# Kernel tuning notes

Hardware: AMD Instinct MI355X
Metric: run time of the kernel (lower is better)

The kernel has to match this reference:

```python
import jax, jax.numpy as jnp
import numpy as np
from jax import lax

NUM_EXPERT = 2   # top-k experts kept per image
N_EXPERTS = 4    # total experts


def setup_inputs() -> dict:
    key = jax.random.key(0)
    ks = jax.random.split(key, 4)
    B, C, H, W = 16, 64, 128, 128
    inputs = jax.random.normal(ks[0], (B, C, H, W), dtype=jnp.float32)
    k = jax.random.uniform(ks[1], (B, C, 1, 1), dtype=jnp.float32)
    gate_w = jax.random.normal(ks[2], (N_EXPERTS, C), dtype=jnp.float32) * (1.0 / np.sqrt(C))
    gate_b = jnp.zeros((N_EXPERTS,), dtype=jnp.float32)
    conv_w = jax.random.normal(ks[3], (N_EXPERTS, C, C, 3, 3), dtype=jnp.float32) * (1.0 / np.sqrt(C * 9))
    conv_b = jnp.zeros((N_EXPERTS, C), dtype=jnp.float32)
    return {"inputs": inputs, "k": k, "gate_w": gate_w, "gate_b": gate_b,
            "conv_w": conv_w, "conv_b": conv_b}


def _expert(x, k, w, b):
    # expert_i(x, k) = ReLU(Conv3x3_i(x) + b_i) * k   (FiLM-style conditioning)
    y = lax.conv_general_dilated(x, w, window_strides=(1, 1), padding='SAME',
                                 dimension_numbers=('NCHW', 'OIHW', 'NCHW'))
    return jax.nn.relu(y + b[None, :, None, None]) * k


def reference(inputs, k, gate_w, gate_b, conv_w, conv_b):
    B = inputs.shape[0]
    # gate: global average pool over HW, then linear C -> E
    pooled = inputs.mean(axis=(2, 3))                       # [B, C]
    logits = pooled @ gate_w.T + gate_b                     # [B, E]
    # softmax in float32 (matches F.softmax(..., dtype=torch.float))
    weights = jax.nn.softmax(logits.astype(jnp.float32), axis=1).astype(inputs.dtype)
    topk_w, topk_idx = lax.top_k(weights, NUM_EXPERT)       # [B, num_expert]
    # scatter top-k weights into a dense [B, E] mask (zeros elsewhere)
    exp_weights = jnp.zeros_like(weights).at[jnp.arange(B)[:, None], topk_idx].set(topk_w)
    # dense loop over ALL experts, weighted sum with mostly-zero weights
    out = inputs
    for i in range(N_EXPERTS):
        out = out + _expert(inputs, k, conv_w[i], conv_b[i]) * exp_weights[:, i, None, None, None]
    return out
```

## Files before the change

### kernel.cpp

```cpp
#include <hip/hip_runtime.h>

typedef __attribute__((ext_vector_type(8))) short bfrag8;
typedef __attribute__((ext_vector_type(4))) short bfrag4;
typedef __attribute__((ext_vector_type(16))) float f32x16;

#define B_ 16
#define C_ 64
#define H_ 128
#define W_ 128
#define E_ 4
#define HW_ (H_ * W_)

#define PLANE 2080
#define ROWB  16640
#define RGK 4

#define WT_ELEMS (4 * 9 * 2 * 4 * 64 * 8)
#define OFF_POOL (WT_ELEMS * 2)
#define OFF_EW   (OFF_POOL + 1024 * 4)
#define WS_NEEDED ((size_t)(OFF_EW + 64 * 4))

#define FB_WT_OFF 0
#define FB_POOLED_OFF 147456
#define FB_EW_OFF 148480

__device__ inline unsigned short f2bf(float f) {
    unsigned u = __builtin_bit_cast(unsigned, f);
    unsigned r = u + 0x7FFFu + ((u >> 16) & 1u);
    return (unsigned short)(r >> 16);
}
__device__ inline float bf2f(unsigned short s) {
    return __builtin_bit_cast(float, (unsigned)s << 16);
}

__global__ __launch_bounds__(256) void pool_wcvt(const float* __restrict__ in,
                                                 const float* __restrict__ cw,
                                                 float* __restrict__ pooled,
                                                 unsigned short* __restrict__ wT2) {
    if (blockIdx.x < 576) {
        const int idx = blockIdx.x * 256 + threadIdx.x;
        const int j = idx & 7;
        const int l = (idx >> 3) & 63;
        const int f = idx >> 9;
        const int kb = f & 3;
        const int chh = (f >> 2) & 1;
        const int et = f >> 3;
        const int tap = et % 9;
        const int e = et / 9;
        const int co = chh * 32 + (l & 31);
        const int ci = kb * 16 + (l >> 5) * 8 + j;
        wT2[idx] = f2bf(cw[(((e * C_ + co) * C_ + ci) * 9) + tap]);
    }
    const int bc = blockIdx.x;
    const float* p = in + (size_t)bc * HW_;
    float s = 0.f;
    for (int i = threadIdx.x; i < HW_ / 4; i += 256) {
        float4 v = ((const float4*)p)[i];
        s += v.x + v.y + v.z + v.w;
    }
    for (int off = 32; off; off >>= 1) s += __shfl_down(s, off);
    __shared__ float red[4];
    const int lane = threadIdx.x & 63, wv = threadIdx.x >> 6;
    if (lane == 0) red[wv] = s;
    __syncthreads();
    if (threadIdx.x == 0)
        pooled[bc] = (red[0] + red[1] + red[2] + red[3]) * (1.0f / (float)HW_);
}

__global__ void gate_kernel(const float* __restrict__ pooled,
                            const float* __restrict__ gate_w,
                            const float* __restrict__ gate_b,
                            float* __restrict__ ew) {
    const int b = threadIdx.x;
    if (b >= B_) return;
    float lg[E_];
    for (int e = 0; e < E_; e++) {
        float s = gate_b[e];
        for (int c = 0; c < C_; c++) s += pooled[b * C_ + c] * gate_w[e * C_ + c];
        lg[e] = s;
    }
    float m = fmaxf(fmaxf(lg[0], lg[1]), fmaxf(lg[2], lg[3]));
    float ex[E_], sum = 0.f;
    for (int e = 0; e < E_; e++) { ex[e] = expf(lg[e] - m); sum += ex[e]; }
    for (int e = 0; e < E_; e++) ex[e] /= sum;
    int i1 = 0;
    for (int e = 1; e < E_; e++) if (ex[e] > ex[i1]) i1 = e;
    int i2 = -1;
    for (int e = 0; e < E_; e++) {
        if (e == i1) continue;
        if (i2 < 0 || ex[e] > ex[i2]) i2 = e;
    }
    for (int e = 0; e < E_; e++)
        ew[b * E_ + e] = (e == i1 || e == i2) ? ex[e] : 0.f;
}

__global__ __launch_bounds__(256, 1) void conv_y(const float* __restrict__ in,
                                                 const float* __restrict__ kk,
                                                 const float* __restrict__ cb,
                                                 const float* __restrict__ pooled,
                                                 const float* __restrict__ gw,
                                                 const float* __restrict__ gb,
                                                 const unsigned short* __restrict__ wT2,
                                                 float* __restrict__ out) {
    const int raw = blockIdx.x;
    const int swz = (raw & 7) * 64 + (raw >> 3);
    const int b   = swz >> 5;
    const int h0  = (swz & 31) * RGK;

    const int tid = threadIdx.x;
    const int lane = tid & 63;
    const int wv = tid >> 6;
    const int ln = lane & 31;
    const int lh = lane >> 5;
    const int ch = wv & 1;
    const int co0 = ch * 32;
    const int x0 = (wv >> 1) * 64;

    const int px = tid & 127;
    const int cset = tid >> 7;

    __shared__ __align__(16) char ring[3 * ROWB];
    __shared__ float sEW[E_];

    if (tid < 64) {
        const float p = pooled[b * C_ + lane];
        float part[E_];
#pragma unroll
        for (int e = 0; e < E_; e++) part[e] = p * gw[e * C_ + lane];
#pragma unroll
        for (int off = 32; off; off >>= 1)
#pragma unroll
            for (int e = 0; e < E_; e++) part[e] += __shfl_down(part[e], off);
        if (lane == 0) {
            float lg[E_];
#pragma unroll
            for (int e = 0; e < E_; e++) lg[e] = part[e] + gb[e];
            float m = fmaxf(fmaxf(lg[0], lg[1]), fmaxf(lg[2], lg[3]));
            float ex[E_], sum = 0.f;
#pragma unroll
            for (int e = 0; e < E_; e++) { ex[e] = __expf(lg[e] - m); sum += ex[e]; }
            const float inv = 1.0f / sum;
            int i1 = 0;
            for (int e = 1; e < E_; e++) if (ex[e] > ex[i1]) i1 = e;
            int i2 = -1;
            for (int e = 0; e < E_; e++) {
                if (e == i1) continue;
                if (i2 < 0 || ex[e] > ex[i2]) i2 = e;
            }
#pragma unroll
            for (int e = 0; e < E_; e++)
                sEW[e] = (e == i1 || e == i2) ? ex[e] * inv : 0.f;
        }
    }
    __syncthreads();

    int e0 = 0, e1 = 0; float w0 = 0.f, w1 = 0.f;
    {
        int found = 0;
        for (int e = 0; e < E_; e++) {
            float we = sEW[e];
            if (we != 0.f) {
                if (!found) { e0 = e; w0 = we; found = 1; }
                else        { e1 = e; w1 = we; }
            }
        }
        if (w1 == 0.f) e1 = e0;
    }

    float pv[32];
    auto STAGE = [&](int r) {
        if ((unsigned)r < (unsigned)H_) {
            const float* src = in + ((size_t)(b * C_ + cset * 32) * H_ + r) * W_ + px;
#pragma unroll
            for (int i = 0; i < 32; ++i) pv[i] = src[(size_t)i * HW_];
        } else {
#pragma unroll
            for (int i = 0; i < 32; ++i) pv[i] = 0.f;
        }
    };
    auto COMMIT = [&](int rs) {
        char* bp = ring + rs * ROWB + (px + 1) * 16;
#pragma unroll
        for (int c4 = 0; c4 < 4; ++c4) {
            bfrag8 f;
#pragma unroll
            for (int j = 0; j < 8; ++j) f[j] = (short)f2bf(pv[c4 * 8 + j]);
            *(bfrag8*)(bp + (cset * 4 + c4) * PLANE) = f;
        }
    };

    if (tid < 48) {
        const int r = tid >> 4;
        const int c = tid & 15;
        const int chh = c >> 1;
        const int sl = (c & 1) ? 129 : 0;
        const bfrag8 z = {0, 0, 0, 0, 0, 0, 0, 0};
        *(bfrag8*)(ring + r * ROWB + chh * PLANE + sl * 16) = z;
    }

    STAGE(h0 - 1); COMMIT(0);
    STAGE(h0);     COMMIT(1);
    STAGE(h0 + 1); COMMIT(2);
    __syncthreads();

    const char* wb0 = (const char*)wT2 + (size_t)e0 * 73728 + ch * 4096 + lane * 16;
    const char* wb1 = (const char*)wT2 + (size_t)e1 * 73728 + ch * 4096 + lane * 16;
    const float* kkp = kk + b * C_;
    const float* cb0 = cb + e0 * C_;
    const float* cb1 = cb + e1 * C_;

    int m0 = 0, m1 = 1, m2 = 2;
    for (int s = 0; s < RGK; ++s) {
        if (s + 1 < RGK) STAGE(h0 + s + 2);

        f32x16 A00, A01, A10, A11;
#pragma unroll
        for (int i = 0; i < 16; ++i) { A00[i] = 0.f; A01[i] = 0.f; A10[i] = 0.f; A11[i] = 0.f; }

#pragma unroll
        for (int ky = 0; ky < 3; ++ky) {
            const char* rb = ring + (ky == 0 ? m0 : (ky == 1 ? m1 : m2)) * ROWB;
#pragma unroll
            for (int kx = 0; kx < 3; ++kx) {
                const int tap = ky * 3 + kx;
#pragma unroll
                for (int kb = 0; kb < 4; ++kb) {
                    bfrag8 a0 = *(const bfrag8*)(wb0 + tap * 8192 + kb * 1024);
                    bfrag8 a1 = *(const bfrag8*)(wb1 + tap * 8192 + kb * 1024);
                    const char* bp = rb + (kb * 2 + lh) * PLANE + (x0 + ln + kx) * 16;
                    bfrag8 b0 = *(const bfrag8*)(bp);
                    bfrag8 b1 = *(const bfrag8*)(bp + 512);
                    A00 = __builtin_amdgcn_mfma_f32_32x32x16_bf16(a0, b0, A00, 0, 0, 0);
                    A01 = __builtin_amdgcn_mfma_f32_32x32x16_bf16(a0, b1, A01, 0, 0, 0);
                    A10 = __builtin_amdgcn_mfma_f32_32x32x16_bf16(a1, b0, A10, 0, 0, 0);
                    A11 = __builtin_amdgcn_mfma_f32_32x32x16_bf16(a1, b1, A11, 0, 0, 0);
                }
            }
        }

        __syncthreads();
        if (s + 1 < RGK) COMMIT(m0);

        const int row = h0 + s;
        const char* rm1 = ring + m1 * ROWB + lh * 8;
        bfrag4 ra0[4], ra1[4];
#pragma unroll
        for (int c = 0; c < 4; ++c) {
            ra0[c] = *(const bfrag4*)(rm1 + (ch * 4 + c) * PLANE + (x0 + ln + 1) * 16);
            ra1[c] = *(const bfrag4*)(rm1 + (ch * 4 + c) * PLANE + (x0 + ln + 33) * 16);
        }
#pragma unroll
        for (int g = 0; g < 16; ++g) {
            const int r_ = g & 3, c_ = g >> 2;
            const int co = co0 + r_ + 8 * c_ + 4 * lh;
            const float kv = kkp[co];
            const float f0 = kv * w0, f1 = kv * w1;
            const float b0v = cb0[co], b1v = cb1[co];
            const size_t base = ((size_t)(b * C_ + co) * H_ + row) * W_;
            out[base + x0 + ln]      = bf2f((unsigned short)ra0[c_][r_])
                                       + fmaxf(A00[g] + b0v, 0.f) * f0
                                       + fmaxf(A10[g] + b1v, 0.f) * f1;
            out[base + x0 + 32 + ln] = bf2f((unsigned short)ra1[c_][r_])
                                       + fmaxf(A01[g] + b0v, 0.f) * f0
                                       + fmaxf(A11[g] + b1v, 0.f) * f1;
        }

        __syncthreads();
        const int t = m0; m0 = m1; m1 = m2; m2 = t;
    }
}

#define CHUNK 32

__global__ __launch_bounds__(256) void pool_kernel(const float* __restrict__ in,
                                                   float* __restrict__ pooled) {
    const int bc = blockIdx.x;
    const float* p = in + (size_t)bc * HW_;
    float s = 0.f;
    for (int i = threadIdx.x; i < HW_ / 4; i += 256) {
        float4 v = ((const float4*)p)[i];
        s += v.x + v.y + v.z + v.w;
    }
    for (int off = 32; off; off >>= 1) s += __shfl_down(s, off);
    __shared__ float red[4];
    const int lane = threadIdx.x & 63, wv = threadIdx.x >> 6;
    if (lane == 0) red[wv] = s;
    __syncthreads();
    if (threadIdx.x == 0)
        pooled[bc] = (red[0] + red[1] + red[2] + red[3]) * (1.0f / (float)HW_);
}

__global__ __launch_bounds__(256) void wtr_kernel(const float* __restrict__ cw,
                                                  float* __restrict__ wT) {
    const int idx = blockIdx.x * 256 + threadIdx.x;
    if (idx >= E_ * C_ * 9 * C_) return;
    const int co = idx & 63;
    const int t2 = idx >> 6;
    const int tap = t2 % 9;
    const int t3 = t2 / 9;
    const int ci = t3 & 63;
    const int e = t3 >> 6;
    wT[idx] = cw[(((e * C_ + co) * C_ + ci) * 9) + tap];
}

__global__ __launch_bounds__(512) void conv_fallback(const float* __restrict__ in,
                                                     const float* __restrict__ kk,
                                                     const float* __restrict__ wT,
                                                     const float* __restrict__ cb,
                                                     const float* __restrict__ ew,
                                                     float* __restrict__ out) {
    const int bid = blockIdx.x;
    const int b = bid / H_;
    const int h = bid % H_;
    const int tid = threadIdx.x;
    const int lane = tid & 63;
    const int wv = tid >> 6;
    const int x0 = wv * 16;

    __shared__ float sIn[CHUNK * 3 * W_];

    float w0 = 0.f, w1 = 0.f;
    int e0 = 0, e1 = 0;
    {
        float we[E_];
#pragma unroll
        for (int e = 0; e < E_; e++) we[e] = ew[b * E_ + e];
        int found = 0;
        for (int e = 0; e < E_; e++) {
            if (we[e] != 0.f) {
                if (!found) { e0 = e; w0 = we[e]; found = 1; }
                else        { e1 = e; w1 = we[e]; }
            }
        }
        if (w1 == 0.f) e1 = e0;
    }

    float acc0[16], acc1[16];
#pragma unroll
    for (int i = 0; i < 16; i++) { acc0[i] = 0.f; acc1[i] = 0.f; }

    for (int cblk = 0; cblk < C_ / CHUNK; cblk++) {
        const int cbase = cblk * CHUNK;
        __syncthreads();
        for (int f = tid; f < CHUNK * 3 * W_ / 4; f += 512) {
            const int fi = f * 4;
            const int ci = fi / (3 * W_);
            const int rem = fi - ci * 3 * W_;
            const int kyy = rem / W_;
            const int x = rem - kyy * W_;
            const int hh = h + kyy - 1;
            float4 v = make_float4(0.f, 0.f, 0.f, 0.f);
            if (hh >= 0 && hh < H_)
                v = *(const float4*)(in + ((size_t)(b * C_ + cbase + ci) * H_ + hh) * W_ + x);
            *(float4*)(sIn + fi) = v;
        }
        __syncthreads();

        const float* wp0 = wT + (size_t)((e0 * C_ + cbase) * 9) * C_ + lane;
        const float* wp1 = wT + (size_t)((e1 * C_ + cbase) * 9) * C_ + lane;
        for (int ci = 0; ci < CHUNK; ci++) {
            float wa[9], wb[9];
#pragma unroll
            for (int t = 0; t < 9; t++) {
                wa[t] = wp0[(ci * 9 + t) * C_];
                wb[t] = wp1[(ci * 9 + t) * C_];
            }
            const float* rowp = sIn + ci * 3 * W_;
#pragma unroll
            for (int kyy = 0; kyy < 3; kyy++) {
                float xin[18];
                const float* rp = rowp + kyy * W_ + x0;
                xin[0] = (x0 == 0) ? 0.f : rp[-1];
#pragma unroll
                for (int j = 0; j < 16; j += 4) {
                    float4 v = *(const float4*)(rp + j);
                    xin[1 + j] = v.x; xin[2 + j] = v.y; xin[3 + j] = v.z; xin[4 + j] = v.w;
                }
                xin[17] = (x0 + 16 >= W_) ? 0.f : rp[16];
                const int t0 = kyy * 3;
#pragma unroll
                for (int x = 0; x < 16; x++) {
                    acc0[x] += xin[x] * wa[t0] + xin[x + 1] * wa[t0 + 1] + xin[x + 2] * wa[t0 + 2];
                    acc1[x] += xin[x] * wb[t0] + xin[x + 1] * wb[t0 + 1] + xin[x + 2] * wb[t0 + 2];
                }
            }
        }
    }

    const float kv = kk[b * C_ + lane];
    const float b0v = cb[e0 * C_ + lane];
    const float b1v = cb[e1 * C_ + lane];
    const float kw0 = kv * w0, kw1 = kv * w1;
    const size_t obase = ((size_t)(b * C_ + lane) * H_ + h) * W_ + x0;
#pragma unroll
    for (int x = 0; x < 16; x += 4) {
        float4 iv = *(const float4*)(in + obase + x);
        float4 ov;
        ov.x = iv.x + fmaxf(acc0[x + 0] + b0v, 0.f) * kw0 + fmaxf(acc1[x + 0] + b1v, 0.f) * kw1;
        ov.y = iv.y + fmaxf(acc0[x + 1] + b0v, 0.f) * kw0 + fmaxf(acc1[x + 1] + b1v, 0.f) * kw1;
        ov.z = iv.z + fmaxf(acc0[x + 2] + b0v, 0.f) * kw0 + fmaxf(acc1[x + 2] + b1v, 0.f) * kw1;
        ov.w = iv.w + fmaxf(acc0[x + 3] + b0v, 0.f) * kw0 + fmaxf(acc1[x + 3] + b1v, 0.f) * kw1;
        *(float4*)(out + obase + x) = ov;
    }
}

extern "C" void kernel_launch(void* const* d_in, const int* in_sizes, int n_in,
                              void* d_out, int out_size, void* d_ws, size_t ws_size,
                              hipStream_t stream) {
    const float* inputs = (const float*)d_in[0];
    const float* k      = (const float*)d_in[1];
    const float* gate_w = (const float*)d_in[2];
    const float* gate_b = (const float*)d_in[3];
    const float* conv_w = (const float*)d_in[4];
    const float* conv_b = (const float*)d_in[5];
    float* out = (float*)d_out;
    char* wsb = (char*)d_ws;

    if (ws_size >= WS_NEEDED) {
        unsigned short* wT2 = (unsigned short*)wsb;
        float* pooled = (float*)(wsb + OFF_POOL);

        pool_wcvt<<<B_ * C_, 256, 0, stream>>>(inputs, conv_w, pooled, wT2);
        conv_y<<<512, 256, 0, stream>>>(inputs, k, conv_b, pooled,
                                        gate_w, gate_b, wT2, out);
    } else {
        float* ws = (float*)d_ws;
        float* wTf    = ws + FB_WT_OFF;
        float* pooled = ws + FB_POOLED_OFF;
        float* ewbuf  = ws + FB_EW_OFF;

        pool_kernel<<<B_ * C_, 256, 0, stream>>>(inputs, pooled);
        gate_kernel<<<1, 64, 0, stream>>>(pooled, gate_w, gate_b, ewbuf);
        wtr_kernel<<<(E_ * C_ * 9 * C_ + 255) / 256, 256, 0, stream>>>(conv_w, wTf);
        conv_fallback<<<B_ * H_, 512, 0, stream>>>(inputs, k, wTf, conv_b, ewbuf, out);
    }
}
```

Before: 84.15 us.

## Split the two selected experts across separate wave groups in conv kernel

The conv kernel now launches 512 threads per block. Waves 0-3 compute expert e0 and waves 4-7 compute expert e1, where before each wave accumulated both experts. Expert-1 waves write their scaled ReLU output to a bf16 shared buffer, and expert-0 waves add it together with the residual and store the result. This halves accumulator registers per wave and doubles the waves available to hide latency. It costs an extra shared-memory round trip, an extra barrier, and bf16 rounding of the second expert's contribution.

```diff
diff --git a/kernel.cpp b/kernel.cpp
--- a/kernel.cpp
+++ b/kernel.cpp
@@ -13,7 +13,7 @@
 
 #define PLANE 2080
 #define ROWB  16640
-#define RGK 4
+#define RG 4
 
 #define WT_ELEMS (4 * 9 * 2 * 4 * 64 * 8)
 #define OFF_POOL (WT_ELEMS * 2)
@@ -94,32 +94,35 @@
         ew[b * E_ + e] = (e == i1 || e == i2) ? ex[e] : 0.f;
 }
 
-__global__ __launch_bounds__(256, 1) void conv_y(const float* __restrict__ in,
-                                                 const float* __restrict__ kk,
-                                                 const float* __restrict__ cb,
-                                                 const float* __restrict__ pooled,
-                                                 const float* __restrict__ gw,
-                                                 const float* __restrict__ gb,
-                                                 const unsigned short* __restrict__ wT2,
-                                                 float* __restrict__ out) {
+__global__ __launch_bounds__(512, 2) void conv_es(const float* __restrict__ in,
+                                                  const float* __restrict__ kk,
+                                                  const float* __restrict__ cb,
+                                                  const float* __restrict__ pooled,
+                                                  const float* __restrict__ gw,
+                                                  const float* __restrict__ gb,
+                                                  const unsigned short* __restrict__ wT2,
+                                                  float* __restrict__ out) {
     const int raw = blockIdx.x;
     const int swz = (raw & 7) * 64 + (raw >> 3);
     const int b   = swz >> 5;
-    const int h0  = (swz & 31) * RGK;
+    const int h0  = (swz & 31) * RG;
 
     const int tid = threadIdx.x;
     const int lane = tid & 63;
     const int wv = tid >> 6;
     const int ln = lane & 31;
     const int lh = lane >> 5;
-    const int ch = wv & 1;
+    const int ei = wv >> 2;
+    const int ch = (wv >> 1) & 1;
+    const int pxh = wv & 1;
     const int co0 = ch * 32;
-    const int x0 = (wv >> 1) * 64;
+    const int x0 = pxh * 64;
 
     const int px = tid & 127;
-    const int cset = tid >> 7;
+    const int cg = tid >> 7;
 
     __shared__ __align__(16) char ring[3 * ROWB];
+    __shared__ unsigned short pbuf16[2 * 2 * 32 * 64];
     __shared__ float sEW[E_];
 
     if (tid < 64) {
@@ -167,26 +170,32 @@
         if (w1 == 0.f) e1 = e0;
     }
 
-    float pv[32];
+    const int es = ei ? e1 : e0;
+    const float ww = ei ? w1 : w0;
+    const float* cbp = cb + es * C_;
+    const float* kkp = kk + b * C_;
+
+    float pv[16];
     auto STAGE = [&](int r) {
         if ((unsigned)r < (unsigned)H_) {
-            const float* src = in + ((size_t)(b * C_ + cset * 32) * H_ + r) * W_ + px;
-#pragma unroll
-            for (int i = 0; i < 32; ++i) pv[i] = src[(size_t)i * HW_];
+            const float* src = in + ((size_t)(b * C_ + cg * 16) * H_ + r) * W_ + px;
+#pragma unroll
+            for (int i = 0; i < 16; ++i) pv[i] = src[(size_t)i * HW_];
         } else {
 #pragma unroll
-            for (int i = 0; i < 32; ++i) pv[i] = 0.f;
+            for (int i = 0; i < 16; ++i) pv[i] = 0.f;
         }
     };
     auto COMMIT = [&](int rs) {
+        bfrag8 f0, f1;
+#pragma unroll
+        for (int j = 0; j < 8; ++j) {
+            f0[j] = (short)f2bf(pv[j]);
+            f1[j] = (short)f2bf(pv[8 + j]);
+        }
         char* bp = ring + rs * ROWB + (px + 1) * 16;
-#pragma unroll
-        for (int c4 = 0; c4 < 4; ++c4) {
-            bfrag8 f;
-#pragma unroll
-            for (int j = 0; j < 8; ++j) f[j] = (short)f2bf(pv[c4 * 8 + j]);
-            *(bfrag8*)(bp + (cset * 4 + c4) * PLANE) = f;
-        }
+        *(bfrag8*)(bp + (cg * 2) * PLANE) = f0;
+        *(bfrag8*)(bp + (cg * 2 + 1) * PLANE) = f1;
     };
 
     if (tid < 48) {
@@ -203,19 +212,16 @@
     STAGE(h0 + 1); COMMIT(2);
     __syncthreads();
 
-    const char* wb0 = (const char*)wT2 + (size_t)e0 * 73728 + ch * 4096 + lane * 16;
-    const char* wb1 = (const char*)wT2 + (size_t)e1 * 73728 + ch * 4096 + lane * 16;
-    const float* kkp = kk + b * C_;
-    const float* cb0 = cb + e0 * C_;
-    const float* cb1 = cb + e1 * C_;
+    const char* wb = (const char*)wT2 + (size_t)es * 73728 + ch * 4096 + lane * 16;
+    unsigned short* pb16 = pbuf16 + (ch * 2 + pxh) * 2048;
 
     int m0 = 0, m1 = 1, m2 = 2;
-    for (int s = 0; s < RGK; ++s) {
-        if (s + 1 < RGK) STAGE(h0 + s + 2);
-
-        f32x16 A00, A01, A10, A11;
-#pragma unroll
-        for (int i = 0; i < 16; ++i) { A00[i] = 0.f; A01[i] = 0.f; A10[i] = 0.f; A11[i] = 0.f; }
+    for (int s = 0; s < RG; ++s) {
+        if (s + 1 < RG) STAGE(h0 + s + 2);
+
+        f32x16 A0, A1;
+#pragma unroll
+        for (int i = 0; i < 16; ++i) { A0[i] = 0.f; A1[i] = 0.f; }
 
 #pragma unroll
         for (int ky = 0; ky < 3; ++ky) {
@@ -225,47 +231,56 @@
                 const int tap = ky * 3 + kx;
 #pragma unroll
                 for (int kb = 0; kb < 4; ++kb) {
-                    bfrag8 a0 = *(const bfrag8*)(wb0 + tap * 8192 + kb * 1024);
-                    bfrag8 a1 = *(const bfrag8*)(wb1 + tap * 8192 + kb * 1024);
+                    bfrag8 a = *(const bfrag8*)(wb + tap * 8192 + kb * 1024);
                     const char* bp = rb + (kb * 2 + lh) * PLANE + (x0 + ln + kx) * 16;
                     bfrag8 b0 = *(const bfrag8*)(bp);
                     bfrag8 b1 = *(const bfrag8*)(bp + 512);
-                    A00 = __builtin_amdgcn_mfma_f32_32x32x16_bf16(a0, b0, A00, 0, 0, 0);
-                    A01 = __builtin_amdgcn_mfma_f32_32x32x16_bf16(a0, b1, A01, 0, 0, 0);
-                    A10 = __builtin_amdgcn_mfma_f32_32x32x16_bf16(a1, b0, A10, 0, 0, 0);
-                    A11 = __builtin_amdgcn_mfma_f32_32x32x16_bf16(a1, b1, A11, 0, 0, 0);
+                    A0 = __builtin_amdgcn_mfma_f32_32x32x16_bf16(a, b0, A0, 0, 0, 0);
+                    A1 = __builtin_amdgcn_mfma_f32_32x32x16_bf16(a, b1, A1, 0, 0, 0);
                 }
             }
         }
 
         __syncthreads();
-        if (s + 1 < RGK) COMMIT(m0);
+        if (s + 1 < RG) COMMIT(m0);
 
         const int row = h0 + s;
-        const char* rm1 = ring + m1 * ROWB + lh * 8;
-        bfrag4 ra0[4], ra1[4];
-#pragma unroll
-        for (int c = 0; c < 4; ++c) {
-            ra0[c] = *(const bfrag4*)(rm1 + (ch * 4 + c) * PLANE + (x0 + ln + 1) * 16);
-            ra1[c] = *(const bfrag4*)(rm1 + (ch * 4 + c) * PLANE + (x0 + ln + 33) * 16);
-        }
-#pragma unroll
-        for (int g = 0; g < 16; ++g) {
-            const int r_ = g & 3, c_ = g >> 2;
-            const int co = co0 + r_ + 8 * c_ + 4 * lh;
-            const float kv = kkp[co];
-            const float f0 = kv * w0, f1 = kv * w1;
-            const float b0v = cb0[co], b1v = cb1[co];
-            const size_t base = ((size_t)(b * C_ + co) * H_ + row) * W_;
-            out[base + x0 + ln]      = bf2f((unsigned short)ra0[c_][r_])
-                                       + fmaxf(A00[g] + b0v, 0.f) * f0
-                                       + fmaxf(A10[g] + b1v, 0.f) * f1;
-            out[base + x0 + 32 + ln] = bf2f((unsigned short)ra1[c_][r_])
-                                       + fmaxf(A01[g] + b0v, 0.f) * f0
-                                       + fmaxf(A11[g] + b1v, 0.f) * f1;
-        }
-
+        if (ei == 1) {
+#pragma unroll
+            for (int g = 0; g < 16; ++g) {
+                const int cs = (g & 3) + 8 * (g >> 2) + 4 * lh;
+                const int co = co0 + cs;
+                const float kvw = kkp[co] * ww;
+                const float cbv = cbp[co];
+                pb16[cs * 64 + ln]      = f2bf(fmaxf(A0[g] + cbv, 0.f) * kvw);
+                pb16[cs * 64 + 32 + ln] = f2bf(fmaxf(A1[g] + cbv, 0.f) * kvw);
+            }
+        }
         __syncthreads();
+        if (ei == 0) {
+            const char* rm1 = ring + m1 * ROWB + lh * 8;
+            bfrag4 ra0[4], ra1[4];
+#pragma unroll
+            for (int c = 0; c < 4; ++c) {
+                ra0[c] = *(const bfrag4*)(rm1 + (ch * 4 + c) * PLANE + (x0 + ln + 1) * 16);
+                ra1[c] = *(const bfrag4*)(rm1 + (ch * 4 + c) * PLANE + (x0 + ln + 33) * 16);
+            }
+#pragma unroll
+            for (int g = 0; g < 16; ++g) {
+                const int r_ = g & 3, c_ = g >> 2;
+                const int cs = r_ + 8 * c_ + 4 * lh;
+                const int co = co0 + cs;
+                const float kvw = kkp[co] * ww;
+                const float cbv = cbp[co];
+                const size_t base = ((size_t)(b * C_ + co) * H_ + row) * W_ + x0;
+                out[base + ln]      = bf2f((unsigned short)ra0[c_][r_])
+                                      + fmaxf(A0[g] + cbv, 0.f) * kvw
+                                      + bf2f(pb16[cs * 64 + ln]);
+                out[base + 32 + ln] = bf2f((unsigned short)ra1[c_][r_])
+                                      + fmaxf(A1[g] + cbv, 0.f) * kvw
+                                      + bf2f(pb16[cs * 64 + 32 + ln]);
+            }
+        }
         const int t = m0; m0 = m1; m1 = m2; m2 = t;
     }
 }
@@ -421,8 +436,8 @@
         float* pooled = (float*)(wsb + OFF_POOL);
 
         pool_wcvt<<<B_ * C_, 256, 0, stream>>>(inputs, conv_w, pooled, wT2);
-        conv_y<<<512, 256, 0, stream>>>(inputs, k, conv_b, pooled,
-                                        gate_w, gate_b, wT2, out);
+        conv_es<<<512, 512, 0, stream>>>(inputs, k, conv_b, pooled,
+                                         gate_w, gate_b, wT2, out);
     } else {
         float* ws = (float*)d_ws;
         float* wTf    = ws + FB_WT_OFF;
```

After: 82.92 us. No clear change (-1.5%).
